# Kernel optimization log

Measured on AMD Instinct MI355X. Metric: run time of the kernel, lower is better.

## Reference

```python
import jax, jax.numpy as jnp
import numpy as np


def _make_constraint_mask(n=9):
    N = n * n
    rows = np.arange(N) // n
    cols = np.arange(N) % n
    box = (rows // 3) * 3 + cols // 3
    cm = np.stack([
        rows[:, None] == rows[None, :],
        cols[:, None] == cols[None, :],
        box[:, None] == box[None, :],
    ], axis=1).astype(np.float32)  # (N, 3, N)
    return cm


def setup_inputs() -> dict:
    n, H, B = 9, 100, 512
    N = n * n
    key = jax.random.key(0)
    k1, k2, k3, k4 = jax.random.split(key, 4)
    digits = jax.random.randint(k1, (B, N), 0, n)
    keep = jax.random.bernoulli(k2, 0.5, (B, N)).astype(jnp.float32)
    x = jax.nn.one_hot(digits, n, dtype=jnp.float32) * keep[..., None]
    constraint_mask = jnp.asarray(_make_constraint_mask(n))  # (81, 3, 81)
    W1 = jax.random.normal(k3, (H, 3 * n), jnp.float32) / np.sqrt(3 * n).astype(np.float32)
    W2 = jax.random.normal(k4, (n, H), jnp.float32) / np.sqrt(H).astype(np.float32)
    return {"x": x, "constraint_mask": constraint_mask, "W1": W1, "W2": W2}


def reference(x, constraint_mask, W1, W2):
    B, N, n = x.shape
    bidx = jnp.arange(B)

    def step(carry, _):
        x, x_pred = carry
        # sparse constraint aggregation: constraints[b,i,k,v] = sum_j cm[i,k,j] * x[b,j,v]
        constraints = jnp.einsum('ikj,bjv->bikv', constraint_mask, x)  # (B,N,3,n)
        empty = x.sum(-1) == 0  # (B,N) cells still unfilled
        f = constraints.reshape(B, N, 3 * n)
        s_ = jax.nn.softmax(jax.nn.relu(f @ W1.T) @ W2.T, axis=-1)  # (B,N,n)
        x_pred = jnp.where(empty[..., None], s_, x_pred)
        s = jnp.where(empty[..., None], s_, 0.0)
        score = s.max(-1)          # (B,N)
        pos = s.argmax(-1)         # (B,N) best digit per cell
        mmax = jnp.argmax(score, axis=1)  # (B,) most confident cell
        has_empty = empty.any(axis=1)     # rows with remaining empties get a write
        p = pos[bidx, mmax]
        old = x[bidx, mmax, p]
        x = x.at[bidx, mmax, p].set(jnp.where(has_empty, 1.0, old))
        return (x, x_pred), None

    # Original loops min_empty (= max empties in batch) times; iterations past a
    # row's fill point are exact no-ops, so a fixed N=n*n steps gives identical output.
    (x, x_pred), _ = jax.lax.scan(step, (x, x), None, length=N)
    return (x_pred, x)
```

## Files before the change

### kernel.cpp

```cpp
#include <hip/hip_runtime.h>
#include <math.h>


#define NCELL 81
#define ND 9
#define NH 100
#define NG 27
#define GP 12
#define W2P 108
#define NTHREADS 256

template<int OFF>
__device__ __forceinline__ float pt_dot(const float* __restrict__ gr,
                                        const float (&w1r)[NG], int bp)
{
    float g[9];
    float4 ga = *(const float4*)gr;
    float4 gb = *(const float4*)(gr + 4);
    g[0]=ga.x; g[1]=ga.y; g[2]=ga.z; g[3]=ga.w;
    g[4]=gb.x; g[5]=gb.y; g[6]=gb.z; g[7]=gb.w;
    g[8]=gr[8];
    float acc = 0.0f;
    #pragma unroll
    for (int v = 0; v < 9; ++v)
        acc = fmaf(w1r[OFF + v], g[v] + ((v == bp) ? 1.0f : 0.0f), acc);
    return acc;
}

__global__ __launch_bounds__(NTHREADS, 2)
void sudoku_solver_kernel(const float* __restrict__ x_in,
                          const float* __restrict__ W1,
                          const float* __restrict__ W2,
                          float* __restrict__ out,
                          int B)
{
    __shared__ float xs[NCELL * ND];
    __shared__ float xp[NCELL * ND];
    alignas(16) __shared__ float gsum[NG * GP];
    alignas(16) __shared__ float PT[NG * NH];
    alignas(16) __shared__ float hs[NCELL * NH];
    alignas(16) __shared__ float W2s[ND * W2P];
    __shared__ unsigned long long pkey[NCELL];
    __shared__ int ecell[NCELL];
    __shared__ int wlist[NCELL];
    __shared__ int EcntS;

    const int b   = blockIdx.x;
    const int tid = threadIdx.x;
    if (b >= B) return;

    const int lane = tid & 63;
    const int wv   = tid >> 6;
    const int sgrp = lane / 9;
    const int vd   = lane - 9 * sgrp;
    const int u    = tid % NH;
    const int sub  = tid / NH;

    float w1r[NG];
    if (tid < 2 * NH) {
        #pragma unroll
        for (int k = 0; k < NG; ++k) w1r[k] = W1[u * NG + k];
    }
    for (int i = tid; i < ND * NH; i += NTHREADS) {
        int row = i / NH, col = i - row * NH;
        W2s[row * W2P + col] = W2[i];
    }
    {
        const float* xb = x_in + (size_t)b * (NCELL * ND);
        for (int i = tid; i < NCELL * ND; i += NTHREADS) {
            float v = xb[i];
            xs[i] = v;
            xp[i] = v;
        }
    }
    for (int i = tid; i < NCELL; i += NTHREADS) pkey[i] = 0ULL;
    if (tid == 0) EcntS = 0;
    __syncthreads();

    for (int t = tid; t < NCELL + NG * ND; t += NTHREADS) {
        if (t < NCELL) {
            const float* r = &xs[t * ND];
            float s = r[0]+r[1]+r[2]+r[3]+r[4]+r[5]+r[6]+r[7]+r[8];
            if (s == 0.0f) {
                int e = atomicAdd(&EcntS, 1);
                int rr = t / 9, cc = t % 9, bb = (rr / 3) * 3 + cc / 3;
                ecell[e] = t | (rr << 8) | (cc << 12) | (bb << 16);
                wlist[e] = t | (e << 8);
            }
        } else {
            int g = (t - NCELL) / ND;
            int v = (t - NCELL) % ND;
            float acc = 0.0f;
            if (g < 9) {
                int base = g * 9;
                #pragma unroll
                for (int j = 0; j < 9; ++j) acc += xs[(base + j) * ND + v];
            } else if (g < 18) {
                int c = g - 9;
                #pragma unroll
                for (int j = 0; j < 9; ++j) acc += xs[(j * 9 + c) * ND + v];
            } else {
                int bb = g - 18;
                int br = (bb / 3) * 3, bc2 = (bb % 3) * 3;
                #pragma unroll
                for (int j = 0; j < 9; ++j)
                    acc += xs[((br + j / 3) * 9 + (bc2 + j % 3)) * ND + v];
            }
            gsum[g * GP + v] = acc;
        }
    }
    __syncthreads();

    int E_live = EcntS;
    int W_reg  = E_live;
    if (tid < 2 * NH) {
        for (int g = sub; g < NG; g += 2) {
            float acc;
            if (g < 9)       acc = pt_dot<0>(&gsum[g * GP], w1r, -1);
            else if (g < 18) acc = pt_dot<9>(&gsum[g * GP], w1r, -1);
            else             acc = pt_dot<18>(&gsum[g * GP], w1r, -1);
            PT[g * NH + u] = acc;
        }
    }
    __syncthreads();

    int pend_cell = -1, pend_digit = 0, pend_be = 0;

    while (E_live > 0) {
        if (tid == NTHREADS - 1 && pend_cell >= 0) {
            int fr = pend_cell / 9, fc = pend_cell % 9;
            int fb = (fr / 3) * 3 + fc / 3;
            xs[pend_cell * ND + pend_digit] = 1.0f;
            gsum[fr * GP + pend_digit]        += 1.0f;
            gsum[(9 + fc) * GP + pend_digit]  += 1.0f;
            gsum[(18 + fb) * GP + pend_digit] += 1.0f;
            pkey[pend_be] = 0ULL;
        }
        for (int ch = tid; ch < W_reg * 25; ch += NTHREADS) {
            int wi = ch / 25, qc = ch - 25 * wi;
            int cell = wlist[wi] & 255;
            int r = cell / 9, c = cell - 9 * r;
            int bg = 18 + (r / 3) * 3 + c / 3;
            float4 hr = ((const float4*)&PT[r * NH])[qc];
            float4 hc = ((const float4*)&PT[(9 + c) * NH])[qc];
            float4 hb = ((const float4*)&PT[bg * NH])[qc];
            float4 h;
            h.x = fmaxf((hr.x + hc.x) + hb.x, 0.0f);
            h.y = fmaxf((hr.y + hc.y) + hb.y, 0.0f);
            h.z = fmaxf((hr.z + hc.z) + hb.z, 0.0f);
            h.w = fmaxf((hr.w + hc.w) + hb.w, 0.0f);
            ((float4*)&hs[wi * NH])[qc] = h;
        }
        __syncthreads();

        const int npass = (W_reg + 27) / 28;
        for (int p = 0; p < npass; ++p) {
            int ci = p * 28 + wv * 7 + sgrp;
            if (sgrp < 7 && ci < W_reg) {
                int went = wlist[ci];
                int cell = went & 255;
                int we   = went >> 8;
                const float4* h4 = (const float4*)&hs[ci * NH];
                const float4* w4 = (const float4*)&W2s[vd * W2P];
                float a0 = 0.0f, a1 = 0.0f;
                #pragma unroll
                for (int q = 0; q < 25; ++q) {
                    float4 hv = h4[q], w = w4[q];
                    a0 = fmaf(w.x, hv.x, a0);
                    a0 = fmaf(w.y, hv.y, a0);
                    a1 = fmaf(w.z, hv.z, a1);
                    a1 = fmaf(w.w, hv.w, a1);
                }
                float l_own = a0 + a1;
                float l[9];
                #pragma unroll
                for (int j = 0; j < 9; ++j) l[j] = __shfl(l_own, 9 * sgrp + j, 64);
                float m = -INFINITY;
                #pragma unroll
                for (int j = 0; j < 9; ++j) m = fmaxf(m, l[j]);
                float e9[9]; float ss = 0.0f;
                #pragma unroll
                for (int j = 0; j < 9; ++j) { e9[j] = expf(l[j] - m); ss += e9[j]; }
                float bestE = -1.0f; int bp = 0;
                #pragma unroll
                for (int j = 0; j < 9; ++j)
                    if (e9[j] > bestE) { bestE = e9[j]; bp = j; }
                xp[cell * ND + vd] = e9[vd] / ss;
                if (vd == 0) {
                    float score = e9[bp] / ss;
                    unsigned lo = ((unsigned)(NCELL - cell) << 11)
                                | ((unsigned)bp << 7) | (unsigned)we;
                    pkey[we] = ((unsigned long long)__float_as_uint(score) << 32) | lo;
                }
            }
        }
        __syncthreads();

        unsigned long long key = 0ULL;
        for (int e = lane; e < NCELL; e += 64) {
            unsigned long long k = pkey[e];
            if (k > key) key = k;
        }
        #pragma unroll
        for (int off = 32; off > 0; off >>= 1) {
            unsigned long long ok = __shfl_xor(key, off, 64);
            if (ok > key) key = ok;
        }
        const unsigned lo = (unsigned)key;
        const int be = (int)(lo & 127);
        const int bp = (int)((lo >> 7) & 15);
        const int bc = NCELL - (int)((lo >> 11) & 127);
        const int fr = bc / 9, fc = bc % 9, fb = (fr / 3) * 3 + fc / 3;

        int Wn = 0;
        for (int base = 0; base < NCELL; base += 64) {
            int e = base + lane;
            bool pr = false; int ce = 0;
            if (e < NCELL && e != be && pkey[e] != 0ULL) {
                int info = ecell[e];
                ce = info & 255;
                int r = (info >> 8) & 15, c = (info >> 12) & 15, bb = (info >> 16) & 15;
                pr = (r == fr) || (c == fc) || (bb == fb);
            }
            unsigned long long mask = __ballot(pr);
            if (wv == 0 && pr) {
                int pos = Wn + (int)__popcll(mask & ((1ULL << lane) - 1ULL));
                wlist[pos] = ce | (e << 8);
            }
            Wn += (int)__popcll(mask);
        }

        if (tid < 2 * NH) {
            if (sub == 0) {
                PT[fr * NH + u]        = pt_dot<0>(&gsum[fr * GP], w1r, bp);
                PT[(18 + fb) * NH + u] = pt_dot<18>(&gsum[(18 + fb) * GP], w1r, bp);
            } else {
                PT[(9 + fc) * NH + u]  = pt_dot<9>(&gsum[(9 + fc) * GP], w1r, bp);
            }
        }

        E_live -= 1;
        pend_cell = bc; pend_digit = bp; pend_be = be;
        W_reg = Wn;
        __syncthreads();
    }

    if (tid == NTHREADS - 1 && pend_cell >= 0)
        xs[pend_cell * ND + pend_digit] = 1.0f;
    __syncthreads();

    const size_t outb = (size_t)b * (NCELL * ND);
    const size_t half = (size_t)B * (NCELL * ND);
    for (int i = tid; i < NCELL * ND; i += NTHREADS) {
        out[outb + i]        = xp[i];
        out[half + outb + i] = xs[i];
    }
}

extern "C" void kernel_launch(void* const* d_in, const int* in_sizes, int n_in,
                              void* d_out, int out_size, void* d_ws, size_t ws_size,
                              hipStream_t stream)
{
    const float* x  = (const float*)d_in[0];
    const float* W1 = (const float*)d_in[2];
    const float* W2 = (const float*)d_in[3];
    float* out = (float*)d_out;
    const int B = in_sizes[0] / (NCELL * ND);

    sudoku_solver_kernel<<<dim3(B), dim3(NTHREADS), 0, stream>>>(x, W1, W2, out, B);
}
```

Baseline: 221.9 us.

## Compact live empty-cell list with swap-remove and drop shared W2 copy

Replaces the fixed 81-entry 64-bit key array with separate score/meta arrays that are kept compact by swap-removing the filled entry, so the argmax and neighbor scans only cover the live empty cells instead of all 81. The argmax key is rebuilt on the fly from score and meta, and row/col/box are recomputed from the cell index rather than stored. W2 is now read directly from global memory (through cache) instead of being staged in padded LDS, which cuts LDS use and setup work but adds global loads in the logits loop. The slot remapping for the last entry adds bookkeeping that must exactly match the deferred swap.

```diff
diff --git a/kernel.cpp b/kernel.cpp
--- a/kernel.cpp
+++ b/kernel.cpp
@@ -7,7 +7,6 @@
 #define NH 100
 #define NG 27
 #define GP 12
-#define W2P 108
 #define NTHREADS 256
 
 template<int OFF>
@@ -39,11 +38,10 @@
     alignas(16) __shared__ float gsum[NG * GP];
     alignas(16) __shared__ float PT[NG * NH];
     alignas(16) __shared__ float hs[NCELL * NH];
-    alignas(16) __shared__ float W2s[ND * W2P];
-    __shared__ unsigned long long pkey[NCELL];
-    __shared__ int ecell[NCELL];
-    __shared__ int wlist[NCELL];
-    __shared__ int EcntS;
+    __shared__ float sc[NCELL];
+    __shared__ int   meta[NCELL];
+    __shared__ int   wlist[NCELL];
+    __shared__ int   EcntS;
 
     const int b   = blockIdx.x;
     const int tid = threadIdx.x;
@@ -61,10 +59,6 @@
         #pragma unroll
         for (int k = 0; k < NG; ++k) w1r[k] = W1[u * NG + k];
     }
-    for (int i = tid; i < ND * NH; i += NTHREADS) {
-        int row = i / NH, col = i - row * NH;
-        W2s[row * W2P + col] = W2[i];
-    }
     {
         const float* xb = x_in + (size_t)b * (NCELL * ND);
         for (int i = tid; i < NCELL * ND; i += NTHREADS) {
@@ -73,7 +67,6 @@
             xp[i] = v;
         }
     }
-    for (int i = tid; i < NCELL; i += NTHREADS) pkey[i] = 0ULL;
     if (tid == 0) EcntS = 0;
     __syncthreads();
 
@@ -83,8 +76,7 @@
             float s = r[0]+r[1]+r[2]+r[3]+r[4]+r[5]+r[6]+r[7]+r[8];
             if (s == 0.0f) {
                 int e = atomicAdd(&EcntS, 1);
-                int rr = t / 9, cc = t % 9, bb = (rr / 3) * 3 + cc / 3;
-                ecell[e] = t | (rr << 8) | (cc << 12) | (bb << 16);
+                meta[e]  = t;
                 wlist[e] = t | (e << 8);
             }
         } else {
@@ -134,7 +126,8 @@
             gsum[fr * GP + pend_digit]        += 1.0f;
             gsum[(9 + fc) * GP + pend_digit]  += 1.0f;
             gsum[(18 + fb) * GP + pend_digit] += 1.0f;
-            pkey[pend_be] = 0ULL;
+            sc[pend_be]   = sc[E_live];
+            meta[pend_be] = meta[E_live];
         }
         for (int ch = tid; ch < W_reg * 25; ch += NTHREADS) {
             int wi = ch / 25, qc = ch - 25 * wi;
@@ -159,9 +152,9 @@
             if (sgrp < 7 && ci < W_reg) {
                 int went = wlist[ci];
                 int cell = went & 255;
-                int we   = went >> 8;
+                int we   = (went >> 8) & 127;
                 const float4* h4 = (const float4*)&hs[ci * NH];
-                const float4* w4 = (const float4*)&W2s[vd * W2P];
+                const float4* w4 = (const float4*)&W2[vd * NH];
                 float a0 = 0.0f, a1 = 0.0f;
                 #pragma unroll
                 for (int q = 0; q < 25; ++q) {
@@ -187,18 +180,23 @@
                     if (e9[j] > bestE) { bestE = e9[j]; bp = j; }
                 xp[cell * ND + vd] = e9[vd] / ss;
                 if (vd == 0) {
-                    float score = e9[bp] / ss;
-                    unsigned lo = ((unsigned)(NCELL - cell) << 11)
-                                | ((unsigned)bp << 7) | (unsigned)we;
-                    pkey[we] = ((unsigned long long)__float_as_uint(score) << 32) | lo;
+                    sc[we]   = e9[bp] / ss;
+                    meta[we] = cell | (bp << 8);
                 }
             }
         }
         __syncthreads();
 
         unsigned long long key = 0ULL;
-        for (int e = lane; e < NCELL; e += 64) {
-            unsigned long long k = pkey[e];
+        for (int e = lane; e < E_live; e += 64) {
+            float s  = sc[e];
+            int   mt = meta[e];
+            int cell = mt & 255;
+            int bpv  = (mt >> 8) & 15;
+            unsigned lo = ((unsigned)(NCELL - cell) << 11)
+                        | ((unsigned)bpv << 7) | (unsigned)e;
+            unsigned long long k =
+                ((unsigned long long)__float_as_uint(s) << 32) | lo;
             if (k > key) key = k;
         }
         #pragma unroll
@@ -213,19 +211,20 @@
         const int fr = bc / 9, fc = bc % 9, fb = (fr / 3) * 3 + fc / 3;
 
         int Wn = 0;
-        for (int base = 0; base < NCELL; base += 64) {
+        for (int base = 0; base < E_live; base += 64) {
             int e = base + lane;
             bool pr = false; int ce = 0;
-            if (e < NCELL && e != be && pkey[e] != 0ULL) {
-                int info = ecell[e];
-                ce = info & 255;
-                int r = (info >> 8) & 15, c = (info >> 12) & 15, bb = (info >> 16) & 15;
+            if (e < E_live && e != be) {
+                ce = meta[e] & 255;
+                int r = ce / 9, c = ce - 9 * r;
+                int bb = (r / 3) * 3 + c / 3;
                 pr = (r == fr) || (c == fc) || (bb == fb);
             }
             unsigned long long mask = __ballot(pr);
             if (wv == 0 && pr) {
-                int pos = Wn + (int)__popcll(mask & ((1ULL << lane) - 1ULL));
-                wlist[pos] = ce | (e << 8);
+                int pos   = Wn + (int)__popcll(mask & ((1ULL << lane) - 1ULL));
+                int slotp = (e == E_live - 1) ? be : e;
+                wlist[pos] = ce | (slotp << 8);
             }
             Wn += (int)__popcll(mask);
         }
```

New measurement: 240.8 us. +8.5%, slower.
